# Kernel optimization log

Hardware: AMD Instinct MI355X
Metric: run time of the kernel (lower is better)

The kernel has to match this reference:

```python
import jax, jax.numpy as jnp
import numpy as np

B, S, D, H = 4, 2048, 1024, 16
DH = D // H
LN_EPS = 1e-5


def setup_inputs() -> dict:
    key = jax.random.key(0)
    ks = jax.random.split(key, 12)
    scale = 0.02
    inp = {
        "x": jax.random.normal(ks[0], (B, S, D), dtype=jnp.float32),
        "attention_mask": jnp.ones((B, 1, 1, S), dtype=jnp.int32),
        # Linear weights stored torch-style: (out_features, in_features)
        "Wq": jax.random.normal(ks[1], (D, D), dtype=jnp.float32) * scale,
        "bq": jax.random.normal(ks[2], (D,), dtype=jnp.float32) * scale,
        "Wk": jax.random.normal(ks[3], (D, D), dtype=jnp.float32) * scale,
        "bk": jax.random.normal(ks[4], (D,), dtype=jnp.float32) * scale,
        "Wv": jax.random.normal(ks[5], (D, D), dtype=jnp.float32) * scale,
        "bv": jax.random.normal(ks[6], (D,), dtype=jnp.float32) * scale,
        "Wo": jax.random.normal(ks[7], (D, D), dtype=jnp.float32) * scale,
        "bo": jax.random.normal(ks[8], (D,), dtype=jnp.float32) * scale,
        "ln_w": jnp.ones((D,), dtype=jnp.float32),
        "ln_b": jnp.zeros((D,), dtype=jnp.float32),
    }
    return inp


def reference(x, attention_mask, Wq, bq, Wk, bk, Wv, bv, Wo, bo, ln_w, ln_b):
    b, s, d = x.shape
    # QKV projections (torch Linear: x @ W.T + b), split into heads -> [b, h, s, dh]
    def proj(W, bias):
        y = jnp.einsum('bsd,ed->bse', x, W) + bias
        return y.reshape(b, s, H, DH).transpose(0, 2, 1, 3)
    q = proj(Wq, bq)
    k = proj(Wk, bk)
    v = proj(Wv, bv)

    scores = jnp.einsum('bhqd,bhkd->bhqk', q, k) / jnp.sqrt(jnp.float32(DH))
    scores = jnp.where(attention_mask == 0, -jnp.inf, scores)
    # max-subtract softmax (stable), identical to jax.nn.softmax
    attn = jax.nn.softmax(scores, axis=-1)
    Hctx = jnp.einsum('bhqk,bhkd->bhqd', attn, v)  # [b, h, s, dh]
    Hctx = Hctx.transpose(0, 2, 1, 3).reshape(b, s, d)

    Hout = jnp.einsum('bsd,ed->bse', Hctx, Wo) + bo
    resid = x + Hout
    mu = jnp.mean(resid, axis=-1, keepdims=True)
    var = jnp.mean(jnp.square(resid - mu), axis=-1, keepdims=True)
    out = (resid - mu) / jnp.sqrt(var + LN_EPS) * ln_w + ln_b
    return out
```

## Files before the change

kernel.cpp:

```cpp
#include <hip/hip_runtime.h>
#include <hip/hip_bf16.h>
#include <stdint.h>

#define Bx  4
#define Sx  2048
#define Dx  1024
#define Hx  16
#define DHx 64
#define Mx  (Bx*Sx)

typedef short bf16x8 __attribute__((ext_vector_type(8)));
typedef float f32x4  __attribute__((ext_vector_type(4)));
typedef float f32x16 __attribute__((ext_vector_type(16)));

#define C1 0.18033688f

__device__ __forceinline__ unsigned short f2bf_u(float f) {
  union { float f; unsigned int u; } c; c.f = f;
  return (unsigned short)((c.u + 0x7fffu + ((c.u >> 16) & 1u)) >> 16);
}
__device__ __forceinline__ unsigned int pack2(float lo, float hi) {
  return ((unsigned int)f2bf_u(hi) << 16) | (unsigned int)f2bf_u(lo);
}
__device__ __forceinline__ unsigned int cvtpk(float lo_, float hi_) {
  unsigned int r;
  asm("v_cvt_pk_bf16_f32 %0, %1, %2" : "=v"(r) : "v"(lo_), "v"(hi_));
  return r;
}
__device__ __forceinline__ void swap32(unsigned int& d, unsigned int& s) {
  asm("v_permlane32_swap_b32 %0, %1" : "+v"(d), "+v"(s));
}

#define GLDS16(gp, lp) __builtin_amdgcn_global_load_lds( \
  (const __attribute__((address_space(1))) unsigned int*)(gp), \
  (__attribute__((address_space(3))) unsigned int*)(lp), 16, 0, 0)

__global__ __launch_bounds__(256) void prep_kernel(
    const float* __restrict__ x,  const float* __restrict__ Wq,
    const float* __restrict__ Wk, const float* __restrict__ Wv,
    const float* __restrict__ Wo, const int* __restrict__ mask,
    uint4* __restrict__ xb4, uint4* __restrict__ wb4,
    float* __restrict__ madd, unsigned* __restrict__ mb) {
  int bid = blockIdx.x, t = threadIdx.x;
  if (bid < 6144) {
    const float* src;
    uint4* dst;
    int i;
    if (bid < 4096) {
      src = x; dst = xb4; i = bid * 256 + t;
    } else {
      int wbid = bid - 4096;
      int widx = wbid >> 9;
      src = (widx == 0) ? Wq : (widx == 1) ? Wk : (widx == 2) ? Wv : Wo;
      dst = wb4 + (size_t)widx * 131072;
      i = (wbid & 511) * 256 + t;
    }
    const float4* s = (const float4*)src + (size_t)i * 2;
    float4 a = s[0], b = s[1];
    uint4 o;
    o.x = pack2(a.x, a.y); o.y = pack2(a.z, a.w);
    o.z = pack2(b.x, b.y); o.w = pack2(b.z, b.w);
    dst[i] = o;
  } else if (bid < 6176) {
    int i = (bid - 6144) * 256 + t;
    madd[i] = (mask[i] == 0) ? -1e30f : 0.0f;
  } else {
    int b = bid - 6176;
    if (t < 64) {
      int any = 0;
      if (t < 32) {
        for (int i = 0; i < 64; ++i) any |= (mask[b * Sx + t * 64 + i] == 0);
      }
      unsigned long long bits = __ballot(any != 0);
      if (t == 0) mb[b] = (unsigned)bits;
    }
  }
}

__global__ __launch_bounds__(256) void qkv_gemm(
    const short* __restrict__ xb, const short* __restrict__ wb,
    const float* __restrict__ bq, const float* __restrict__ bk,
    const float* __restrict__ bv,
    short* __restrict__ qb, short* __restrict__ kb, short* __restrict__ vb) {
  int lid = blockIdx.x + (blockIdx.y << 3) + (blockIdx.z << 9);
  int xcd = lid & 7;
  int idx = lid >> 3;
  int which = idx >> 6;
  int tt = idx & 63;
  int m0 = (xcd * 8 + (tt >> 3)) * 128;
  int n0 = (tt & 7) * 128;

  const short* Wm  = wb + (size_t)which * Dx * Dx;
  const float* bias = (which == 0) ? bq : (which == 1 ? bk : bv);

  __shared__ alignas(16) short smem[128 * 136];
  short* Al = smem;
  short* Bl = smem + 4096;

  int t = threadIdx.x;
  int l = t & 63, w = t >> 6;
  int wm = w >> 1, wn = w & 1;
  int srow = l >> 2;
  int scol = (l & 3) * 8;
  int fr = l & 15, fg = l >> 4;

  f32x4 acc[4][4] = {};

  for (int k0 = 0; k0 < Dx; k0 += 32) {
#pragma unroll
    for (int i = 0; i < 2; ++i) {
      int r0 = (w * 2 + i) * 16;
      const short* ga = xb + (size_t)(m0 + r0 + srow) * Dx + k0 + scol;
      GLDS16(ga, &Al[r0 * 32]);
      const short* gb = Wm + (size_t)(n0 + r0 + srow) * Dx + k0 + scol;
      GLDS16(gb, &Bl[r0 * 32]);
    }
    __syncthreads();
    bf16x8 af[4], bfm[4];
#pragma unroll
    for (int i = 0; i < 4; ++i)
      af[i] = *(const bf16x8*)&Al[(wm * 64 + i * 16 + fr) * 32 + fg * 8];
#pragma unroll
    for (int i = 0; i < 4; ++i)
      bfm[i] = *(const bf16x8*)&Bl[(wn * 64 + i * 16 + fr) * 32 + fg * 8];
#pragma unroll
    for (int mi = 0; mi < 4; ++mi)
#pragma unroll
      for (int ni = 0; ni < 4; ++ni)
        acc[mi][ni] = __builtin_amdgcn_mfma_f32_16x16x32_bf16(
            af[mi], bfm[ni], acc[mi][ni], 0, 0, 0);
    __syncthreads();
  }

  if (which == 2) {
#pragma unroll
    for (int ni = 0; ni < 4; ++ni) {
      int n_l = wn * 64 + ni * 16 + fr;
      float bias_n = bias[n0 + n_l];
#pragma unroll
      for (int mi = 0; mi < 4; ++mi)
#pragma unroll
        for (int r = 0; r < 4; ++r) {
          int m_l = wm * 64 + mi * 16 + fg * 4 + r;
          smem[n_l * 136 + m_l] = (short)f2bf_u(acc[mi][ni][r] + bias_n);
        }
    }
    __syncthreads();
    int b = m0 >> 11, s0_ = m0 & 2047;
#pragma unroll
    for (int it = 0; it < 8; ++it) {
      int idx2 = t + it * 256;
      int n_l = idx2 >> 4, c = idx2 & 15;
      int4 v = *(const int4*)&smem[n_l * 136 + c * 8];
      int n = n0 + n_l, h = n >> 6, dh = n & 63;
      int chunk = (c & 7) ^ (dh & 7);
      size_t off = (size_t)(b * Hx + h) * Sx * 64
                 + (size_t)((s0_ >> 6) + (c >> 3)) * 4096
                 + dh * 64 + chunk * 8;
      *(int4*)&vb[off] = v;
    }
    return;
  }

#pragma unroll
  for (int ni = 0; ni < 4; ++ni) {
    int n = n0 + wn * 64 + ni * 16 + fr;
    int h = n >> 6, dh = n & 63;
    float bias_n = bias[n];
#pragma unroll
    for (int mi = 0; mi < 4; ++mi) {
#pragma unroll
      for (int r = 0; r < 4; ++r) {
        int m = m0 + wm * 64 + mi * 16 + fg * 4 + r;
        int b = m >> 11, s = m & 2047;
        float y = acc[mi][ni][r] + bias_n;
        size_t hb = (size_t)(b * Hx + h) * Sx * DHx;
        if (which == 0) {
          qb[hb + (size_t)s * DHx + dh] = (short)f2bf_u(y * C1);
        } else {
          kb[hb + (size_t)s * 64 + ((((dh >> 3) ^ (s & 7)) << 3) | (dh & 7))] =
              (short)f2bf_u(y);
        }
      }
    }
  }
}

__global__ __launch_bounds__(256) void attn_kernel(
    const short* __restrict__ qb, const short* __restrict__ kb,
    const short* __restrict__ vb, const float* __restrict__ madd,
    const unsigned* __restrict__ maskbits, short* __restrict__ cbuf) {
  int bh = blockIdx.x;
  int qt = blockIdx.y;
  int b  = bh >> 4;

  __shared__ alignas(16) short Kl[2][4096];
  __shared__ alignas(16) short Vt[2][4096];

  int t = threadIdx.x, l = t & 63, w = t >> 6;
  int lo = l & 31, hi = l >> 5;

  const short* qg = qb + ((size_t)bh * Sx + qt * 128 + w * 32 + lo) * 64;
  bf16x8 qf[4];
#pragma unroll
  for (int ks = 0; ks < 4; ++ks)
    qf[ks] = *(const bf16x8*)&qg[ks * 16 + hi * 8];

  int koff[4], koff32[4];
#pragma unroll
  for (int ks = 0; ks < 4; ++ks) {
    int c = ((2 * ks + hi) ^ (lo & 7)) << 3;
    koff[ks]   = lo * 64 + c;
    koff32[ks] = (32 + lo) * 64 + c;
  }

  const short* kg = kb + (size_t)bh * Sx * 64;
  const short* vg = vb + (size_t)bh * Sx * 64;
  const float* mg = madd + b * Sx;
  unsigned mbits = maskbits[b];

  bf16x8 ones;
#pragma unroll
  for (int i = 0; i < 8; ++i) ones[i] = (short)0x3F80;

  f32x16 O0 = {}, O1 = {}, Ssum = {};

#define STAGE(tile, bf) do {                                              \
    const short* ks_ = kg + (size_t)(tile) * 4096;                        \
    const short* vs_ = vg + (size_t)(tile) * 4096;                        \
    GLDS16(ks_ + w * 512 + l * 8,        &Kl[bf][w * 512]);               \
    GLDS16(ks_ + 2048 + w * 512 + l * 8, &Kl[bf][2048 + w * 512]);        \
    GLDS16(vs_ + w * 512 + l * 8,        &Vt[bf][w * 512]);               \
    GLDS16(vs_ + 2048 + w * 512 + l * 8, &Vt[bf][2048 + w * 512]);        \
  } while (0)

#define TBODY(tile, cur) do {                                             \
    if ((tile) < 31) {                                                    \
      STAGE((tile) + 1, (cur) ^ 1);                                       \
      asm volatile("s_waitcnt vmcnt(4)" ::: "memory");                    \
    } else {                                                              \
      asm volatile("s_waitcnt vmcnt(0)" ::: "memory");                    \
    }                                                                     \
    __builtin_amdgcn_s_barrier();                                         \
    const short* Kb = &Kl[cur][0];                                        \
    const short* Vb = &Vt[cur][0];                                        \
    f32x16 st0 = {}, st1 = {};                                            \
    __builtin_amdgcn_s_setprio(1);                                        \
    _Pragma("unroll")                                                     \
    for (int ks = 0; ks < 4; ++ks)                                        \
      st0 = __builtin_amdgcn_mfma_f32_32x32x16_bf16(                      \
          *(const bf16x8*)&Kb[koff[ks]], qf[ks], st0, 0, 0, 0);           \
    _Pragma("unroll")                                                     \
    for (int ks = 0; ks < 4; ++ks)                                        \
      st1 = __builtin_amdgcn_mfma_f32_32x32x16_bf16(                      \
          *(const bf16x8*)&Kb[koff32[ks]], qf[ks], st1, 0, 0, 0);         \
    __builtin_amdgcn_s_setprio(0);                                        \
    if ((mbits >> (tile)) & 1) {                                          \
      const float* mrow = mg + (tile) * 64;                               \
      _Pragma("unroll")                                                   \
      for (int r = 0; r < 16; ++r) {                                      \
        int key = (r & 3) + 8 * (r >> 2) + 4 * hi;                        \
        st0[r] += mrow[key];                                              \
        st1[r] += mrow[32 + key];                                         \
      }                                                                   \
    }                                                                     \
    _Pragma("unroll")                                                     \
    for (int r = 0; r < 16; ++r) {                                        \
      st0[r] = __builtin_amdgcn_exp2f(st0[r]);                            \
      st1[r] = __builtin_amdgcn_exp2f(st1[r]);                            \
    }                                                                     \
    __builtin_amdgcn_s_setprio(1);                                        \
    _Pragma("unroll")                                                     \
    for (int kbi = 0; kbi < 2; ++kbi) {                                   \
      _Pragma("unroll")                                                   \
      for (int half = 0; half < 2; ++half) {                              \
        int po = half * 8;                                                \
        unsigned int u, u2, v, v2;                                        \
        if (kbi == 0) {                                                   \
          u  = cvtpk(st0[po + 0], st0[po + 1]);                           \
          u2 = cvtpk(st0[po + 2], st0[po + 3]);                           \
          v  = cvtpk(st0[po + 4], st0[po + 5]);                           \
          v2 = cvtpk(st0[po + 6], st0[po + 7]);                           \
        } else {                                                          \
          u  = cvtpk(st1[po + 0], st1[po + 1]);                           \
          u2 = cvtpk(st1[po + 2], st1[po + 3]);                           \
          v  = cvtpk(st1[po + 4], st1[po + 5]);                           \
          v2 = cvtpk(st1[po + 6], st1[po + 7]);                           \
        }                                                                 \
        swap32(v, u);                                                     \
        swap32(v2, u2);                                                   \
        union { unsigned int i[4]; bf16x8 v8; } pu;                       \
        pu.i[0] = u; pu.i[1] = u2; pu.i[2] = v; pu.i[3] = v2;             \
        int vi = kbi * 2 + half;                                          \
        bf16x8 vf0 = *(const bf16x8*)&Vb[koff[vi]];                       \
        bf16x8 vf1 = *(const bf16x8*)&Vb[koff32[vi]];                     \
        O0 = __builtin_amdgcn_mfma_f32_32x32x16_bf16(pu.v8, vf0, O0, 0, 0, 0);   \
        O1 = __builtin_amdgcn_mfma_f32_32x32x16_bf16(pu.v8, vf1, O1, 0, 0, 0);   \
        Ssum = __builtin_amdgcn_mfma_f32_32x32x16_bf16(pu.v8, ones, Ssum, 0, 0, 0); \
      }                                                                   \
    }                                                                     \
    __builtin_amdgcn_s_setprio(0);                                        \
    __builtin_amdgcn_s_barrier();                                         \
  } while (0)

  STAGE(0, 0);

  for (int tile = 0; tile < 32; tile += 2) {
    TBODY(tile, 0);
    TBODY(tile + 1, 1);
  }
#undef TBODY
#undef STAGE

  int h = bh & 15, bq_ = bh >> 4;
#pragma unroll
  for (int a = 0; a < 4; ++a) {
#pragma unroll
    for (int j = 0; j < 4; ++j) {
      int r = a * 4 + j;
      float linv = __builtin_amdgcn_rcpf(Ssum[r]);
      int s = qt * 128 + w * 32 + a * 8 + hi * 4 + j;
      size_t rowb = ((size_t)(bq_ * Sx + s)) * Dx + h * 64;
      cbuf[rowb + lo]      = (short)f2bf_u(O0[r] * linv);
      cbuf[rowb + 32 + lo] = (short)f2bf_u(O1[r] * linv);
    }
  }
}

__global__ __launch_bounds__(256) void proj_gemm(
    const short* __restrict__ cb, const short* __restrict__ wo,
    const float* __restrict__ bo, const float* __restrict__ x,
    float* __restrict__ out) {
  int lid = blockIdx.x + (blockIdx.y << 3);
  int xcd = lid & 7;
  int tt = lid >> 3;
  int m0 = (xcd * 8 + (tt >> 3)) * 128;
  int n0 = (tt & 7) * 128;

  __shared__ alignas(16) short Al[128 * 32];
  __shared__ alignas(16) short Bl[128 * 32];

  int t = threadIdx.x;
  int l = t & 63, w = t >> 6;
  int wm = w >> 1, wn = w & 1;
  int srow = l >> 2, scol = (l & 3) * 8;
  int fr = l & 15, fg = l >> 4;

  f32x4 acc[4][4] = {};

  for (int k0 = 0; k0 < Dx; k0 += 32) {
#pragma unroll
    for (int i = 0; i < 2; ++i) {
      int r0 = (w * 2 + i) * 16;
      const short* ga = cb + (size_t)(m0 + r0 + srow) * Dx + k0 + scol;
      GLDS16(ga, &Al[r0 * 32]);
      const short* gb = wo + (size_t)(n0 + r0 + srow) * Dx + k0 + scol;
      GLDS16(gb, &Bl[r0 * 32]);
    }
    __syncthreads();
    bf16x8 af[4], bfm[4];
#pragma unroll
    for (int i = 0; i < 4; ++i)
      af[i] = *(const bf16x8*)&Al[(wm * 64 + i * 16 + fr) * 32 + fg * 8];
#pragma unroll
    for (int i = 0; i < 4; ++i)
      bfm[i] = *(const bf16x8*)&Bl[(wn * 64 + i * 16 + fr) * 32 + fg * 8];
#pragma unroll
    for (int mi = 0; mi < 4; ++mi)
#pragma unroll
      for (int ni = 0; ni < 4; ++ni)
        acc[mi][ni] = __builtin_amdgcn_mfma_f32_16x16x32_bf16(
            af[mi], bfm[ni], acc[mi][ni], 0, 0, 0);
    __syncthreads();
  }

#pragma unroll
  for (int ni = 0; ni < 4; ++ni) {
    int n = n0 + wn * 64 + ni * 16 + fr;
    float bias_n = bo[n];
#pragma unroll
    for (int mi = 0; mi < 4; ++mi) {
#pragma unroll
      for (int r = 0; r < 4; ++r) {
        int m = m0 + wm * 64 + mi * 16 + fg * 4 + r;
        float y = acc[mi][ni][r] + bias_n + x[(size_t)m * Dx + n];
        out[(size_t)m * Dx + n] = y;
      }
    }
  }
}

__global__ __launch_bounds__(256) void ln_kernel(float* __restrict__ io,
                                                 const float* __restrict__ lw,
                                                 const float* __restrict__ lb) {
  int row = blockIdx.x;
  float* p = io + (size_t)row * Dx;
  int c = threadIdx.x * 4;
  float4 v = *(float4*)&p[c];
  float s = v.x + v.y + v.z + v.w;
  float q = v.x * v.x + v.y * v.y + v.z * v.z + v.w * v.w;
#pragma unroll
  for (int d = 1; d < 64; d <<= 1) {
    s += __shfl_xor(s, d, 64);
    q += __shfl_xor(q, d, 64);
  }
  __shared__ float ss[4], qq[4];
  int l = threadIdx.x & 63, w = threadIdx.x >> 6;
  if (l == 0) { ss[w] = s; qq[w] = q; }
  __syncthreads();
  s = ss[0] + ss[1] + ss[2] + ss[3];
  q = qq[0] + qq[1] + qq[2] + qq[3];
  float mu = s * (1.f / Dx);
  float var = q * (1.f / Dx) - mu * mu;
  float rstd = rsqrtf(var + 1e-5f);
  float4 w4 = *(const float4*)&lw[c];
  float4 b4 = *(const float4*)&lb[c];
  float4 o;
  o.x = (v.x - mu) * rstd * w4.x + b4.x;
  o.y = (v.y - mu) * rstd * w4.y + b4.y;
  o.z = (v.z - mu) * rstd * w4.z + b4.z;
  o.w = (v.w - mu) * rstd * w4.w + b4.w;
  *(float4*)&p[c] = o;
}

extern "C" void kernel_launch(void* const* d_in, const int* in_sizes, int n_in,
                              void* d_out, int out_size, void* d_ws, size_t ws_size,
                              hipStream_t stream) {
  const float* x   = (const float*)d_in[0];
  const int*   msk = (const int*)d_in[1];
  const float* Wq  = (const float*)d_in[2];
  const float* bq  = (const float*)d_in[3];
  const float* Wk  = (const float*)d_in[4];
  const float* bk  = (const float*)d_in[5];
  const float* Wv  = (const float*)d_in[6];
  const float* bv  = (const float*)d_in[7];
  const float* Wo  = (const float*)d_in[8];
  const float* bo  = (const float*)d_in[9];
  const float* lnw = (const float*)d_in[10];
  const float* lnb = (const float*)d_in[11];
  float* out = (float*)d_out;

  char* ws = (char*)d_ws;
  short* xb = (short*)(ws);
  short* wb = (short*)(ws + (size_t)(16 << 20));
  short* qb = (short*)(ws + (size_t)(24 << 20));
  short* kb = (short*)(ws + (size_t)(40 << 20));
  short* vb = (short*)(ws + (size_t)(56 << 20));
  short* cb = (short*)(ws + (size_t)(72 << 20));
  float* madd = out;
  unsigned* mbits = (unsigned*)(out + Mx);

  prep_kernel<<<6180, 256, 0, stream>>>(x, Wq, Wk, Wv, Wo, msk,
                                        (uint4*)xb, (uint4*)wb, madd, mbits);
  qkv_gemm<<<dim3(8, 64, 3), 256, 0, stream>>>(xb, wb, bq, bk, bv, qb, kb, vb);
  attn_kernel<<<dim3(64, 16), 256, 0, stream>>>(qb, kb, vb, madd, mbits, cb);
  proj_gemm<<<dim3(8, 64), 256, 0, stream>>>(cb, wb + 3 * (size_t)(Dx * Dx), bo, x, out);
  ln_kernel<<<Mx, 256, 0, stream>>>(out, lnw, lnb);
}
```

Baseline: 219.9 us.

## Process two query sub-tiles per attention wave to reuse K/V fragments

Each wave now handles 64 query rows, split into two 32-row groups A and B, instead of 32. Each K and V fragment read from LDS feeds MFMAs for both groups, and each CTA covers 256 queries, which halves the grid and the K/V global staging per query. The cost is roughly double the accumulator and score registers per thread, which may force lower occupancy or spills; launch_bounds(256,2) is added to steer register allocation. The grid also shrinks to 512 blocks, which can reduce load balance across CUs.

```diff
diff --git a/kernel.cpp b/kernel.cpp
--- a/kernel.cpp
+++ b/kernel.cpp
@@ -186,7 +186,7 @@
   }
 }
 
-__global__ __launch_bounds__(256) void attn_kernel(
+__global__ __launch_bounds__(256, 2) void attn_kernel(
     const short* __restrict__ qb, const short* __restrict__ kb,
     const short* __restrict__ vb, const float* __restrict__ madd,
     const unsigned* __restrict__ maskbits, short* __restrict__ cbuf) {
@@ -200,11 +200,14 @@
   int t = threadIdx.x, l = t & 63, w = t >> 6;
   int lo = l & 31, hi = l >> 5;
 
-  const short* qg = qb + ((size_t)bh * Sx + qt * 128 + w * 32 + lo) * 64;
-  bf16x8 qf[4];
-#pragma unroll
-  for (int ks = 0; ks < 4; ++ks)
-    qf[ks] = *(const bf16x8*)&qg[ks * 16 + hi * 8];
+  const short* qgA = qb + ((size_t)bh * Sx + qt * 256 + w * 64 + lo) * 64;
+  const short* qgB = qgA + 32 * 64;
+  bf16x8 qfA[4], qfB[4];
+#pragma unroll
+  for (int ks = 0; ks < 4; ++ks) {
+    qfA[ks] = *(const bf16x8*)&qgA[ks * 16 + hi * 8];
+    qfB[ks] = *(const bf16x8*)&qgB[ks * 16 + hi * 8];
+  }
 
   int koff[4], koff32[4];
 #pragma unroll
@@ -223,7 +226,8 @@
 #pragma unroll
   for (int i = 0; i < 8; ++i) ones[i] = (short)0x3F80;
 
-  f32x16 O0 = {}, O1 = {}, Ssum = {};
+  f32x16 OA0 = {}, OA1 = {}, SsA = {};
+  f32x16 OB0 = {}, OB1 = {}, SsB = {};
 
 #define STAGE(tile, bf) do {                                              \
     const short* ks_ = kg + (size_t)(tile) * 4096;                        \
@@ -244,30 +248,37 @@
     __builtin_amdgcn_s_barrier();                                         \
     const short* Kb = &Kl[cur][0];                                        \
     const short* Vb = &Vt[cur][0];                                        \
-    f32x16 st0 = {}, st1 = {};                                            \
+    f32x16 sA0 = {}, sA1 = {}, sB0 = {}, sB1 = {};                        \
     __builtin_amdgcn_s_setprio(1);                                        \
     _Pragma("unroll")                                                     \
-    for (int ks = 0; ks < 4; ++ks)                                        \
-      st0 = __builtin_amdgcn_mfma_f32_32x32x16_bf16(                      \
-          *(const bf16x8*)&Kb[koff[ks]], qf[ks], st0, 0, 0, 0);           \
+    for (int ks = 0; ks < 4; ++ks) {                                      \
+      bf16x8 kf = *(const bf16x8*)&Kb[koff[ks]];                          \
+      sA0 = __builtin_amdgcn_mfma_f32_32x32x16_bf16(kf, qfA[ks], sA0, 0, 0, 0); \
+      sB0 = __builtin_amdgcn_mfma_f32_32x32x16_bf16(kf, qfB[ks], sB0, 0, 0, 0); \
+    }                                                                     \
     _Pragma("unroll")                                                     \
-    for (int ks = 0; ks < 4; ++ks)                                        \
-      st1 = __builtin_amdgcn_mfma_f32_32x32x16_bf16(                      \
-          *(const bf16x8*)&Kb[koff32[ks]], qf[ks], st1, 0, 0, 0);         \
+    for (int ks = 0; ks < 4; ++ks) {                                      \
+      bf16x8 kf = *(const bf16x8*)&Kb[koff32[ks]];                        \
+      sA1 = __builtin_amdgcn_mfma_f32_32x32x16_bf16(kf, qfA[ks], sA1, 0, 0, 0); \
+      sB1 = __builtin_amdgcn_mfma_f32_32x32x16_bf16(kf, qfB[ks], sB1, 0, 0, 0); \
+    }                                                                     \
     __builtin_amdgcn_s_setprio(0);                                        \
     if ((mbits >> (tile)) & 1) {                                          \
       const float* mrow = mg + (tile) * 64;                               \
       _Pragma("unroll")                                                   \
       for (int r = 0; r < 16; ++r) {                                      \
         int key = (r & 3) + 8 * (r >> 2) + 4 * hi;                        \
-        st0[r] += mrow[key];                                              \
-        st1[r] += mrow[32 + key];                                         \
+        float m0_ = mrow[key], m1_ = mrow[32 + key];                      \
+        sA0[r] += m0_; sA1[r] += m1_;                                     \
+        sB0[r] += m0_; sB1[r] += m1_;                                     \
       }                                                                   \
     }                                                                     \
     _Pragma("unroll")                                                     \
     for (int r = 0; r < 16; ++r) {                                        \
-      st0[r] = __builtin_amdgcn_exp2f(st0[r]);                            \
-      st1[r] = __builtin_amdgcn_exp2f(st1[r]);                            \
+      sA0[r] = __builtin_amdgcn_exp2f(sA0[r]);                            \
+      sA1[r] = __builtin_amdgcn_exp2f(sA1[r]);                            \
+      sB0[r] = __builtin_amdgcn_exp2f(sB0[r]);                            \
+      sB1[r] = __builtin_amdgcn_exp2f(sB1[r]);                            \
     }                                                                     \
     __builtin_amdgcn_s_setprio(1);                                        \
     _Pragma("unroll")                                                     \
@@ -275,28 +286,40 @@
       _Pragma("unroll")                                                   \
       for (int half = 0; half < 2; ++half) {                              \
         int po = half * 8;                                                \
-        unsigned int u, u2, v, v2;                                        \
+        unsigned int uA, uA2, vA, vA2, uB, uB2, vB, vB2;                  \
         if (kbi == 0) {                                                   \
-          u  = cvtpk(st0[po + 0], st0[po + 1]);                           \
-          u2 = cvtpk(st0[po + 2], st0[po + 3]);                           \
-          v  = cvtpk(st0[po + 4], st0[po + 5]);                           \
-          v2 = cvtpk(st0[po + 6], st0[po + 7]);                           \
+          uA  = cvtpk(sA0[po + 0], sA0[po + 1]);                          \
+          uA2 = cvtpk(sA0[po + 2], sA0[po + 3]);                          \
+          vA  = cvtpk(sA0[po + 4], sA0[po + 5]);                          \
+          vA2 = cvtpk(sA0[po + 6], sA0[po + 7]);                          \
+          uB  = cvtpk(sB0[po + 0], sB0[po + 1]);                          \
+          uB2 = cvtpk(sB0[po + 2], sB0[po + 3]);                          \
+          vB  = cvtpk(sB0[po + 4], sB0[po + 5]);                          \
+          vB2 = cvtpk(sB0[po + 6], sB0[po + 7]);                          \
         } else {                                                          \
-          u  = cvtpk(st1[po + 0], st1[po + 1]);                           \
-          u2 = cvtpk(st1[po + 2], st1[po + 3]);                           \
-          v  = cvtpk(st1[po + 4], st1[po + 5]);                           \
-          v2 = cvtpk(st1[po + 6], st1[po + 7]);                           \
+          uA  = cvtpk(sA1[po + 0], sA1[po + 1]);                          \
+          uA2 = cvtpk(sA1[po + 2], sA1[po + 3]);                          \
+          vA  = cvtpk(sA1[po + 4], sA1[po + 5]);                          \
+          vA2 = cvtpk(sA1[po + 6], sA1[po + 7]);                          \
+          uB  = cvtpk(sB1[po + 0], sB1[po + 1]);                          \
+          uB2 = cvtpk(sB1[po + 2], sB1[po + 3]);                          \
+          vB  = cvtpk(sB1[po + 4], sB1[po + 5]);                          \
+          vB2 = cvtpk(sB1[po + 6], sB1[po + 7]);                          \
         }                                                                 \
-        swap32(v, u);                                                     \
-        swap32(v2, u2);                                                   \
-        union { unsigned int i[4]; bf16x8 v8; } pu;                       \
-        pu.i[0] = u; pu.i[1] = u2; pu.i[2] = v; pu.i[3] = v2;             \
+        swap32(vA, uA); swap32(vA2, uA2);                                 \
+        swap32(vB, uB); swap32(vB2, uB2);                                 \
+        union { unsigned int i[4]; bf16x8 v8; } puA, puB;                 \
+        puA.i[0] = uA; puA.i[1] = uA2; puA.i[2] = vA; puA.i[3] = vA2;     \
+        puB.i[0] = uB; puB.i[1] = uB2; puB.i[2] = vB; puB.i[3] = vB2;     \
         int vi = kbi * 2 + half;                                          \
         bf16x8 vf0 = *(const bf16x8*)&Vb[koff[vi]];                       \
         bf16x8 vf1 = *(const bf16x8*)&Vb[koff32[vi]];                     \
-        O0 = __builtin_amdgcn_mfma_f32_32x32x16_bf16(pu.v8, vf0, O0, 0, 0, 0);   \
-        O1 = __builtin_amdgcn_mfma_f32_32x32x16_bf16(pu.v8, vf1, O1, 0, 0, 0);   \
-        Ssum = __builtin_amdgcn_mfma_f32_32x32x16_bf16(pu.v8, ones, Ssum, 0, 0, 0); \
+        OA0 = __builtin_amdgcn_mfma_f32_32x32x16_bf16(puA.v8, vf0, OA0, 0, 0, 0); \
+        OA1 = __builtin_amdgcn_mfma_f32_32x32x16_bf16(puA.v8, vf1, OA1, 0, 0, 0); \
+        SsA = __builtin_amdgcn_mfma_f32_32x32x16_bf16(puA.v8, ones, SsA, 0, 0, 0); \
+        OB0 = __builtin_amdgcn_mfma_f32_32x32x16_bf16(puB.v8, vf0, OB0, 0, 0, 0); \
+        OB1 = __builtin_amdgcn_mfma_f32_32x32x16_bf16(puB.v8, vf1, OB1, 0, 0, 0); \
+        SsB = __builtin_amdgcn_mfma_f32_32x32x16_bf16(puB.v8, ones, SsB, 0, 0, 0); \
       }                                                                   \
     }                                                                     \
     __builtin_amdgcn_s_setprio(0);                                        \
@@ -318,11 +341,17 @@
 #pragma unroll
     for (int j = 0; j < 4; ++j) {
       int r = a * 4 + j;
-      float linv = __builtin_amdgcn_rcpf(Ssum[r]);
-      int s = qt * 128 + w * 32 + a * 8 + hi * 4 + j;
-      size_t rowb = ((size_t)(bq_ * Sx + s)) * Dx + h * 64;
-      cbuf[rowb + lo]      = (short)f2bf_u(O0[r] * linv);
-      cbuf[rowb + 32 + lo] = (short)f2bf_u(O1[r] * linv);
+      int srow = a * 8 + hi * 4 + j;
+      float linvA = __builtin_amdgcn_rcpf(SsA[r]);
+      float linvB = __builtin_amdgcn_rcpf(SsB[r]);
+      int sA = qt * 256 + w * 64 + srow;
+      int sB = sA + 32;
+      size_t rowbA = ((size_t)(bq_ * Sx + sA)) * Dx + h * 64;
+      size_t rowbB = ((size_t)(bq_ * Sx + sB)) * Dx + h * 64;
+      cbuf[rowbA + lo]      = (short)f2bf_u(OA0[r] * linvA);
+      cbuf[rowbA + 32 + lo] = (short)f2bf_u(OA1[r] * linvA);
+      cbuf[rowbB + lo]      = (short)f2bf_u(OB0[r] * linvB);
+      cbuf[rowbB + 32 + lo] = (short)f2bf_u(OB1[r] * linvB);
     }
   }
 }
@@ -453,7 +482,7 @@
   prep_kernel<<<6180, 256, 0, stream>>>(x, Wq, Wk, Wv, Wo, msk,
                                         (uint4*)xb, (uint4*)wb, madd, mbits);
   qkv_gemm<<<dim3(8, 64, 3), 256, 0, stream>>>(xb, wb, bq, bk, bv, qb, kb, vb);
-  attn_kernel<<<dim3(64, 16), 256, 0, stream>>>(qb, kb, vb, madd, mbits, cb);
+  attn_kernel<<<dim3(64, 8), 256, 0, stream>>>(qb, kb, vb, madd, mbits, cb);
   proj_gemm<<<dim3(8, 64), 256, 0, stream>>>(cb, wb + 3 * (size_t)(Dx * Dx), bo, x, out);
   ln_kernel<<<Mx, 256, 0, stream>>>(out, lnw, lnb);
 }
```

Result: faster. 207.5 us (-5.6%).
